# Optimization experiments

Hardware: AMD Instinct MI355X
Metric: run time of the kernel (lower is better)

## Reference

```python
import jax, jax.numpy as jnp
import numpy as np

N = 3072      # num nodes in g
E = 3072      # num edges in g (= num nodes in line graph lg)
E_LG = 6144   # num edges in line graph
F_NODE = 64
F_EDGE = 64
H = 4         # num_heads


def _init_linear(key, fan_in, fan_out):
    k1, k2 = jax.random.split(key)
    bound = 1.0 / np.sqrt(fan_in).astype(np.float32)
    W = jax.random.uniform(k1, (fan_in, fan_out), minval=-bound, maxval=bound, dtype=jnp.float32)
    b = jax.random.uniform(k2, (fan_out,), minval=-bound, maxval=bound, dtype=jnp.float32)
    return W, b


def setup_inputs() -> dict:
    key = jax.random.key(0)
    ks = jax.random.split(key, 12)
    node_inputs = jax.random.normal(ks[0], (N, F_NODE), dtype=jnp.float32)
    edge_inputs = jax.random.normal(ks[1], (E, F_EDGE), dtype=jnp.float32)
    src = jax.random.randint(ks[2], (E,), 0, N)
    dst = jax.random.randint(ks[3], (E,), 0, N)
    lg_src = jax.random.randint(ks[4], (E_LG,), 0, E)
    lg_dst = jax.random.randint(ks[5], (E_LG,), 0, E)
    nqW, nqb = _init_linear(ks[6], F_NODE, H * F_NODE)
    nkW, nkb = _init_linear(ks[7], F_NODE, H)
    nvW, nvb = _init_linear(ks[8], F_NODE, H * F_NODE)
    eqW, eqb = _init_linear(ks[9], F_EDGE, H * F_EDGE)
    ekW, ekb = _init_linear(ks[10], F_EDGE, H)
    evW, evb = _init_linear(ks[11], F_EDGE, H * F_EDGE)
    return dict(node_inputs=node_inputs, edge_inputs=edge_inputs,
                src=src, dst=dst, lg_src=lg_src, lg_dst=lg_dst,
                nqW=nqW, nqb=nqb, nkW=nkW, nkb=nkb, nvW=nvW, nvb=nvb,
                eqW=eqW, eqb=eqb, ekW=ekW, ekb=ekb, evW=evW, evb=evb)


def _self_attention(query, key_t, feats, short_residual):
    # query [H,M,F], key_t [H,M,1], short_residual [M,F]
    # original: softmax((q @ sr^T @ k) / sqrt(F), dim=1)
    # associate as q @ (sr^T @ k) to avoid an [H,M,M] intermediate
    srk = jnp.einsum('mf,hmo->hfo', short_residual, key_t)          # [H,F,1]
    x = jnp.einsum('hmf,hfo->hmo', query, srk) / np.float32(np.sqrt(feats))
    return jax.nn.softmax(x, axis=1)                                 # [H,M,1]


def reference(node_inputs, edge_inputs, src, dst, lg_src, lg_dst,
              nqW, nqb, nkW, nkb, nvW, nvb, eqW, eqb, ekW, ekb, evW, evb):
    # linear projections; torch .view(H,-1,F) on a row-major [M,H*F] tensor
    # is exactly jnp.reshape((H, M, F))
    node_q = (node_inputs @ nqW + nqb).reshape(H, N, F_NODE)
    node_k = (node_inputs @ nkW + nkb).reshape(H, N, 1)
    node_v = (node_inputs @ nvW + nvb).reshape(H, N, F_NODE)
    edge_q = (edge_inputs @ eqW + eqb).reshape(H, E, F_EDGE)
    edge_k = (edge_inputs @ ekW + ekb).reshape(H, E, 1)
    edge_v = (edge_inputs @ evW + evb).reshape(H, E, F_EDGE)

    node_att = _self_attention(node_q, node_k, F_NODE, node_inputs)  # [H,N,1]
    edge_att = _self_attention(edge_q, edge_k, F_EDGE, edge_inputs)  # [H,E,1]

    # scatter per-edge attention scores into dense [H,N,N]
    node_proj = jnp.zeros((H, N, N), jnp.float32).at[:, src, dst].set(edge_att[:, :, 0])
    # line-graph edge e1 -> e2 passes through connecting node dst[e1]
    conn = dst[lg_src]                                               # [E_LG]
    edge_proj = jnp.zeros((H, E, E), jnp.float32).at[:, lg_src, lg_dst].set(node_att[:, conn, 0])

    # dense adjacency masks
    adj_g = jnp.zeros((N, N), jnp.float32).at[src, dst].set(1.0)
    adj_lg = jnp.zeros((E, E), jnp.float32).at[lg_src, lg_dst].set(1.0)

    # message passing, aggregation='sum': (proj * adj) @ value
    node_msg = jnp.einsum('hnm,hmf->hnf', node_proj * adj_g, node_v)   # [H,N,F]
    edge_msg = jnp.einsum('hnm,hmf->hnf', edge_proj * adj_lg, edge_v)  # [H,E,F]

    # head pooling 'mean' (dropout p=0 => identity)
    return node_msg.mean(axis=0), edge_msg.mean(axis=0)
```

## Files before the change

### kernel.cpp

```cpp
#include <hip/hip_runtime.h>

#define N_NODES 3072
#define N_EDGES 3072
#define N_LG    6144
#define F       64
#define H       4
#define HASH_SZ 16384
#define HASH_MASK (HASH_SZ - 1)

#define OFF_PV   0
#define OFF_SRK  (OFF_PV + 2*H*N_NODES*F)
#define OFF_ATT  (OFF_SRK + 2*H*F)
#define OFF_HASH (OFF_ATT + 2*H*N_NODES)

__global__ __launch_bounds__(256) void init_kernel(
    float4* __restrict__ out, int4* __restrict__ hash, float* __restrict__ srk)
{
    const int b = blockIdx.x, t = threadIdx.x;
    if (b < 384) {
        out[b * 256 + t] = make_float4(0.f, 0.f, 0.f, 0.f);
    } else if (b < 448) {
        const int idx = (b - 384) * 256 + t;
        hash[idx] = (idx < 8192) ? make_int4(-1, -1, -1, -1) : make_int4(0, 0, 0, 0);
    } else {
        srk[t] = 0.f;
        srk[t + 256] = 0.f;
    }
}

__device__ __forceinline__ unsigned hash_slot(unsigned key) {
    return (key * 2654435761u >> 16) & HASH_MASK;
}

__global__ __launch_bounds__(256) void hash_insert_kernel(
    const int* __restrict__ src, const int* __restrict__ dst,
    const int* __restrict__ lg_src, const int* __restrict__ lg_dst,
    unsigned* __restrict__ keys_g, int* __restrict__ vals_g,
    unsigned* __restrict__ keys_lg, int* __restrict__ vals_lg)
{
    int b = blockIdx.x;
    const int* s; const int* d; unsigned* keys; int* vals; int n;
    if (b < 12) { s = src;    d = dst;    keys = keys_g;  vals = vals_g;  n = N_EDGES; }
    else { b -= 12; s = lg_src; d = lg_dst; keys = keys_lg; vals = vals_lg; n = N_LG; }
    const int e = b * 256 + threadIdx.x;
    if (e >= n) return;
    const unsigned key = (unsigned)(s[e] * N_NODES + d[e]);
    unsigned idx = hash_slot(key);
    while (true) {
        unsigned prev = atomicCAS(&keys[idx], 0xFFFFFFFFu, key);
        if (prev == 0xFFFFFFFFu || prev == key) { atomicMax(&vals[idx], e); break; }
        idx = (idx + 1) & HASH_MASK;
    }
}

__device__ __forceinline__ int hash_is_winner(
    unsigned key, const unsigned* __restrict__ keys, const int* __restrict__ vals, int e)
{
    unsigned idx = hash_slot(key);
    while (keys[idx] != key) idx = (idx + 1) & HASH_MASK;
    return vals[idx] == e;
}

__global__ __launch_bounds__(256) void srk_kernel(
    const float* __restrict__ node_in, const float* __restrict__ edge_in,
    const float* __restrict__ nkW, const float* __restrict__ nkb,
    const float* __restrict__ ekW, const float* __restrict__ ekb,
    float* __restrict__ srk)
{
    const int kind = blockIdx.y, b = blockIdx.x, t = threadIdx.x;
    const int h = b / 12, m0 = (b % 12) * 256, r0 = b * 64;
    const float* in = kind ? edge_in : node_in;
    const float* Wk = kind ? ekW : nkW;
    const float* bk = kind ? ekb : nkb;
    __shared__ float sin_[64 * 68];
    __shared__ float k_lds[256];
    __shared__ float wk_s[256];
    __shared__ float bk_s[4];
    #pragma unroll
    for (int i = 0; i < 4; ++i) {
        const int idx = t + i * 256;
        const int m = idx >> 4, q = idx & 15;
        float4 v = ((const float4*)(in + (size_t)(r0 + m) * F))[q];
        *(float4*)&sin_[m * 68 + q * 4] = v;
    }
    wk_s[t] = Wk[t];
    if (t < 4) bk_s[t] = bk[t];
    __syncthreads();
    {
        const int rl = t >> 2, c = t & 3;
        float acc = bk_s[c];
        #pragma unroll
        for (int j = 0; j < F; ++j) acc += sin_[rl * 68 + j] * wk_s[j * 4 + c];
        k_lds[t] = acc;
    }
    __syncthreads();
    {
        const int c = t >> 6, f = t & 63;
        float acc = 0.f;
        const float* base = in + (size_t)(m0 + c * 64) * F + f;
        #pragma unroll
        for (int mp = 0; mp < 64; ++mp) acc += base[(size_t)mp * F] * k_lds[c * 64 + mp];
        atomicAdd(&srk[(kind * H + h) * F + f], acc);
    }
}

__global__ __launch_bounds__(1024) void att_kernel(
    const float* __restrict__ node_in, const float* __restrict__ edge_in,
    const float* __restrict__ nqW, const float* __restrict__ nqb,
    const float* __restrict__ eqW, const float* __restrict__ eqb,
    float* __restrict__ ws)
{
    const int h = blockIdx.x, kind = blockIdx.y, tid = threadIdx.x;
    const float* in = kind ? edge_in : node_in;
    const float* Wq = kind ? eqW : nqW;
    const float* bq = kind ? eqb : nqb;
    float* att = ws + OFF_ATT + (kind * H + h) * N_NODES;
    __shared__ float s_srk[F];
    __shared__ float s_w[256];
    __shared__ float s_beff[4];
    __shared__ float sred[16];
    if (tid < F) s_srk[tid] = ws[OFF_SRK + (kind * H + h) * F + tid];
    __syncthreads();
    if (tid < 256) {
        const int c4 = tid >> 6, j = tid & 63;
        float we = 0.f;
        #pragma unroll
        for (int f = 0; f < F; ++f) we += Wq[j * 256 + c4 * 64 + f] * s_srk[f];
        s_w[c4 * 64 + j] = we;
    } else if (tid < 260) {
        const int c4 = tid - 256;
        float be = 0.f;
        #pragma unroll
        for (int f = 0; f < F; ++f) be += bq[c4 * 64 + f] * s_srk[f];
        s_beff[c4] = be;
    }
    __syncthreads();
    float x[3];
    float mx = -1e30f;
    #pragma unroll
    for (int j = 0; j < 3; ++j) {
        const int m = tid * 3 + j;
        const int row = h * 768 + (m >> 2);
        const int c4 = m & 3;
        const float4* q4 = (const float4*)(in + (size_t)row * F);
        const float* w = s_w + c4 * 64;
        float a = 0.f;
        #pragma unroll
        for (int i = 0; i < 16; ++i) {
            float4 v = q4[i];
            a += v.x * w[i * 4] + v.y * w[i * 4 + 1] + v.z * w[i * 4 + 2] + v.w * w[i * 4 + 3];
        }
        x[j] = (a + s_beff[c4]) * 0.125f;
        mx = fmaxf(mx, x[j]);
    }
    #pragma unroll
    for (int o = 1; o < 64; o <<= 1) mx = fmaxf(mx, __shfl_xor(mx, o));
    const int wid = tid >> 6, lane = tid & 63;
    if (lane == 0) sred[wid] = mx;
    __syncthreads();
    if (tid == 0) { float m2 = sred[0]; for (int i = 1; i < 16; ++i) m2 = fmaxf(m2, sred[i]); sred[0] = m2; }
    __syncthreads();
    mx = sred[0];
    __syncthreads();
    float s = 0.f;
    #pragma unroll
    for (int j = 0; j < 3; ++j) { x[j] = __expf(x[j] - mx); s += x[j]; }
    #pragma unroll
    for (int o = 1; o < 64; o <<= 1) s += __shfl_xor(s, o);
    if (lane == 0) sred[wid] = s;
    __syncthreads();
    if (tid == 0) { float t = 0.f; for (int i = 0; i < 16; ++i) t += sred[i]; sred[0] = t; }
    __syncthreads();
    const float inv = 1.0f / sred[0];
    #pragma unroll
    for (int j = 0; j < 3; ++j) att[tid * 3 + j] = x[j] * inv;
}

__global__ __launch_bounds__(256) void proj_v_kernel(
    const float* __restrict__ node_in, const float* __restrict__ edge_in,
    const float* __restrict__ nvW, const float* __restrict__ nvb,
    const float* __restrict__ evW, const float* __restrict__ evb,
    float* __restrict__ ws)
{
    const int kind = blockIdx.y, col = threadIdx.x;
    const int m0 = blockIdx.x * 32;
    const float* in = kind ? edge_in : node_in;
    const float* W  = kind ? evW : nvW;
    const float* bv = kind ? evb : nvb;
    __shared__ float sin_[32 * 68];
    #pragma unroll
    for (int i = 0; i < 2; ++i) {
        const int idx = col + i * 256;
        const int m = idx >> 4, q = idx & 15;
        float4 v = ((const float4*)(in + (size_t)(m0 + m) * F))[q];
        *(float4*)&sin_[m * 68 + q * 4] = v;
    }
    __syncthreads();
    float acc[32];
    const float b0 = bv[col];
    #pragma unroll
    for (int r = 0; r < 32; ++r) acc[r] = b0;
    #pragma unroll
    for (int k4 = 0; k4 < 16; ++k4) {
        const float w0 = W[(k4 * 4 + 0) * 256 + col];
        const float w1 = W[(k4 * 4 + 1) * 256 + col];
        const float w2 = W[(k4 * 4 + 2) * 256 + col];
        const float w3 = W[(k4 * 4 + 3) * 256 + col];
        #pragma unroll
        for (int r = 0; r < 32; ++r) {
            float4 v = *(const float4*)&sin_[r * 68 + k4 * 4];
            acc[r] = fmaf(v.x, w0, fmaf(v.y, w1, fmaf(v.z, w2, fmaf(v.w, w3, acc[r]))));
        }
    }
    float* V = ws + OFF_PV + (size_t)kind * H * N_NODES * F;
    #pragma unroll
    for (int r = 0; r < 32; ++r)
        V[(size_t)(m0 + r) * 256 + col] = acc[r];
}

__global__ __launch_bounds__(64) void scatter_kernel(
    const int* __restrict__ src, const int* __restrict__ dst,
    const int* __restrict__ lg_src, const int* __restrict__ lg_dst,
    const float* __restrict__ ws,
    const unsigned* __restrict__ keys_g, const int* __restrict__ vals_g,
    const unsigned* __restrict__ keys_lg, const int* __restrict__ vals_lg,
    float* __restrict__ out)
{
    const int b = blockIdx.x;
    const int f = threadIdx.x;
    if (b < N_EDGES) {
        const int e = b;
        const int s = src[e], d = dst[e];
        const unsigned key = (unsigned)(s * N_NODES + d);
        if (!hash_is_winner(key, keys_g, vals_g, e)) return;
        const float* att = ws + OFF_ATT + H * N_NODES;
        const float* V   = ws + OFF_PV;
        float acc = 0.f;
        #pragma unroll
        for (int h = 0; h < H; ++h)
            acc += att[h * N_EDGES + e] * V[(size_t)h * N_NODES * F + (size_t)d * F + f];
        atomicAdd(&out[s * F + f], 0.25f * acc);
    } else {
        const int l = b - N_EDGES;
        const int e1 = lg_src[l], e2 = lg_dst[l];
        const unsigned key = (unsigned)(e1 * N_NODES + e2);
        if (!hash_is_winner(key, keys_lg, vals_lg, l)) return;
        const int conn = dst[e1];
        const float* att = ws + OFF_ATT;
        const float* V   = ws + OFF_PV + (size_t)H * N_EDGES * F;
        float acc = 0.f;
        #pragma unroll
        for (int h = 0; h < H; ++h)
            acc += att[h * N_NODES + conn] * V[(size_t)h * N_EDGES * F + (size_t)e2 * F + f];
        atomicAdd(&out[N_NODES * F + e1 * F + f], 0.25f * acc);
    }
}

extern "C" void kernel_launch(void* const* d_in, const int* in_sizes, int n_in,
                              void* d_out, int out_size, void* d_ws, size_t ws_size,
                              hipStream_t stream)
{
    const float* node_in = (const float*)d_in[0];
    const float* edge_in = (const float*)d_in[1];
    const int* src    = (const int*)d_in[2];
    const int* dst    = (const int*)d_in[3];
    const int* lg_src = (const int*)d_in[4];
    const int* lg_dst = (const int*)d_in[5];
    const float* nqW = (const float*)d_in[6];  const float* nqb = (const float*)d_in[7];
    const float* nkW = (const float*)d_in[8];  const float* nkb = (const float*)d_in[9];
    const float* nvW = (const float*)d_in[10]; const float* nvb = (const float*)d_in[11];
    const float* eqW = (const float*)d_in[12]; const float* eqb = (const float*)d_in[13];
    const float* ekW = (const float*)d_in[14]; const float* ekb = (const float*)d_in[15];
    const float* evW = (const float*)d_in[16]; const float* evb = (const float*)d_in[17];

    float* ws  = (float*)d_ws;
    float* out = (float*)d_out;
    unsigned* keys_g  = (unsigned*)(ws + OFF_HASH);
    unsigned* keys_lg = keys_g + HASH_SZ;
    int* vals_g  = (int*)(keys_g + 2 * HASH_SZ);
    int* vals_lg = vals_g + HASH_SZ;

    hipLaunchKernelGGL(init_kernel, dim3(449), dim3(256), 0, stream,
                       (float4*)out, (int4*)(ws + OFF_HASH), ws + OFF_SRK);
    hipLaunchKernelGGL(hash_insert_kernel, dim3(36), dim3(256), 0, stream,
                       src, dst, lg_src, lg_dst, keys_g, vals_g, keys_lg, vals_lg);
    hipLaunchKernelGGL(srk_kernel, dim3(48, 2), dim3(256), 0, stream,
                       node_in, edge_in, nkW, nkb, ekW, ekb, ws + OFF_SRK);
    hipLaunchKernelGGL(att_kernel, dim3(H, 2), dim3(1024), 0, stream,
                       node_in, edge_in, nqW, nqb, eqW, eqb, ws);
    hipLaunchKernelGGL(proj_v_kernel, dim3(96, 2), dim3(256), 0, stream,
                       node_in, edge_in, nvW, nvb, evW, evb, ws);
    hipLaunchKernelGGL(scatter_kernel, dim3(N_EDGES + N_LG), dim3(64), 0, stream,
                       src, dst, lg_src, lg_dst, ws, keys_g, vals_g, keys_lg, vals_lg, out);
}
```

Before: 150.8 us.

## Fuse all stages into one cooperative persistent kernel with grid syncs

```diff
diff --git a/kernel.cpp b/kernel.cpp
--- a/kernel.cpp
+++ b/kernel.cpp
@@ -1,4 +1,7 @@
 #include <hip/hip_runtime.h>
+#include <hip/hip_cooperative_groups.h>
+
+namespace cg = cooperative_groups;
 
 #define N_NODES 3072
 #define N_EDGES 3072
@@ -13,44 +16,10 @@
 #define OFF_ATT  (OFF_SRK + 2*H*F)
 #define OFF_HASH (OFF_ATT + 2*H*N_NODES)
 
-__global__ __launch_bounds__(256) void init_kernel(
-    float4* __restrict__ out, int4* __restrict__ hash, float* __restrict__ srk)
-{
-    const int b = blockIdx.x, t = threadIdx.x;
-    if (b < 384) {
-        out[b * 256 + t] = make_float4(0.f, 0.f, 0.f, 0.f);
-    } else if (b < 448) {
-        const int idx = (b - 384) * 256 + t;
-        hash[idx] = (idx < 8192) ? make_int4(-1, -1, -1, -1) : make_int4(0, 0, 0, 0);
-    } else {
-        srk[t] = 0.f;
-        srk[t + 256] = 0.f;
-    }
-}
+#define NBLK 256
 
 __device__ __forceinline__ unsigned hash_slot(unsigned key) {
     return (key * 2654435761u >> 16) & HASH_MASK;
-}
-
-__global__ __launch_bounds__(256) void hash_insert_kernel(
-    const int* __restrict__ src, const int* __restrict__ dst,
-    const int* __restrict__ lg_src, const int* __restrict__ lg_dst,
-    unsigned* __restrict__ keys_g, int* __restrict__ vals_g,
-    unsigned* __restrict__ keys_lg, int* __restrict__ vals_lg)
-{
-    int b = blockIdx.x;
-    const int* s; const int* d; unsigned* keys; int* vals; int n;
-    if (b < 12) { s = src;    d = dst;    keys = keys_g;  vals = vals_g;  n = N_EDGES; }
-    else { b -= 12; s = lg_src; d = lg_dst; keys = keys_lg; vals = vals_lg; n = N_LG; }
-    const int e = b * 256 + threadIdx.x;
-    if (e >= n) return;
-    const unsigned key = (unsigned)(s[e] * N_NODES + d[e]);
-    unsigned idx = hash_slot(key);
-    while (true) {
-        unsigned prev = atomicCAS(&keys[idx], 0xFFFFFFFFu, key);
-        if (prev == 0xFFFFFFFFu || prev == key) { atomicMax(&vals[idx], e); break; }
-        idx = (idx + 1) & HASH_MASK;
-    }
 }
 
 __device__ __forceinline__ int hash_is_winner(
@@ -61,198 +30,233 @@
     return vals[idx] == e;
 }
 
-__global__ __launch_bounds__(256) void srk_kernel(
+#define L_SIN   0
+#define L_KL    4352
+#define L_WK    4608
+#define L_BK    4864
+#define L_RED   4868
+#define LDS_FLOATS (L_RED + 16)
+
+__global__ __launch_bounds__(256) void mega_kernel(
     const float* __restrict__ node_in, const float* __restrict__ edge_in,
-    const float* __restrict__ nkW, const float* __restrict__ nkb,
-    const float* __restrict__ ekW, const float* __restrict__ ekb,
-    float* __restrict__ srk)
-{
-    const int kind = blockIdx.y, b = blockIdx.x, t = threadIdx.x;
-    const int h = b / 12, m0 = (b % 12) * 256, r0 = b * 64;
-    const float* in = kind ? edge_in : node_in;
-    const float* Wk = kind ? ekW : nkW;
-    const float* bk = kind ? ekb : nkb;
-    __shared__ float sin_[64 * 68];
-    __shared__ float k_lds[256];
-    __shared__ float wk_s[256];
-    __shared__ float bk_s[4];
-    #pragma unroll
-    for (int i = 0; i < 4; ++i) {
-        const int idx = t + i * 256;
-        const int m = idx >> 4, q = idx & 15;
-        float4 v = ((const float4*)(in + (size_t)(r0 + m) * F))[q];
-        *(float4*)&sin_[m * 68 + q * 4] = v;
-    }
-    wk_s[t] = Wk[t];
-    if (t < 4) bk_s[t] = bk[t];
-    __syncthreads();
-    {
-        const int rl = t >> 2, c = t & 3;
-        float acc = bk_s[c];
-        #pragma unroll
-        for (int j = 0; j < F; ++j) acc += sin_[rl * 68 + j] * wk_s[j * 4 + c];
-        k_lds[t] = acc;
-    }
-    __syncthreads();
-    {
-        const int c = t >> 6, f = t & 63;
-        float acc = 0.f;
-        const float* base = in + (size_t)(m0 + c * 64) * F + f;
-        #pragma unroll
-        for (int mp = 0; mp < 64; ++mp) acc += base[(size_t)mp * F] * k_lds[c * 64 + mp];
-        atomicAdd(&srk[(kind * H + h) * F + f], acc);
-    }
-}
-
-__global__ __launch_bounds__(1024) void att_kernel(
-    const float* __restrict__ node_in, const float* __restrict__ edge_in,
-    const float* __restrict__ nqW, const float* __restrict__ nqb,
-    const float* __restrict__ eqW, const float* __restrict__ eqb,
-    float* __restrict__ ws)
-{
-    const int h = blockIdx.x, kind = blockIdx.y, tid = threadIdx.x;
-    const float* in = kind ? edge_in : node_in;
-    const float* Wq = kind ? eqW : nqW;
-    const float* bq = kind ? eqb : nqb;
-    float* att = ws + OFF_ATT + (kind * H + h) * N_NODES;
-    __shared__ float s_srk[F];
-    __shared__ float s_w[256];
-    __shared__ float s_beff[4];
-    __shared__ float sred[16];
-    if (tid < F) s_srk[tid] = ws[OFF_SRK + (kind * H + h) * F + tid];
-    __syncthreads();
-    if (tid < 256) {
-        const int c4 = tid >> 6, j = tid & 63;
-        float we = 0.f;
-        #pragma unroll
-        for (int f = 0; f < F; ++f) we += Wq[j * 256 + c4 * 64 + f] * s_srk[f];
-        s_w[c4 * 64 + j] = we;
-    } else if (tid < 260) {
-        const int c4 = tid - 256;
-        float be = 0.f;
-        #pragma unroll
-        for (int f = 0; f < F; ++f) be += bq[c4 * 64 + f] * s_srk[f];
-        s_beff[c4] = be;
-    }
-    __syncthreads();
-    float x[3];
-    float mx = -1e30f;
-    #pragma unroll
-    for (int j = 0; j < 3; ++j) {
-        const int m = tid * 3 + j;
-        const int row = h * 768 + (m >> 2);
-        const int c4 = m & 3;
-        const float4* q4 = (const float4*)(in + (size_t)row * F);
-        const float* w = s_w + c4 * 64;
-        float a = 0.f;
-        #pragma unroll
-        for (int i = 0; i < 16; ++i) {
-            float4 v = q4[i];
-            a += v.x * w[i * 4] + v.y * w[i * 4 + 1] + v.z * w[i * 4 + 2] + v.w * w[i * 4 + 3];
-        }
-        x[j] = (a + s_beff[c4]) * 0.125f;
-        mx = fmaxf(mx, x[j]);
-    }
-    #pragma unroll
-    for (int o = 1; o < 64; o <<= 1) mx = fmaxf(mx, __shfl_xor(mx, o));
-    const int wid = tid >> 6, lane = tid & 63;
-    if (lane == 0) sred[wid] = mx;
-    __syncthreads();
-    if (tid == 0) { float m2 = sred[0]; for (int i = 1; i < 16; ++i) m2 = fmaxf(m2, sred[i]); sred[0] = m2; }
-    __syncthreads();
-    mx = sred[0];
-    __syncthreads();
-    float s = 0.f;
-    #pragma unroll
-    for (int j = 0; j < 3; ++j) { x[j] = __expf(x[j] - mx); s += x[j]; }
-    #pragma unroll
-    for (int o = 1; o < 64; o <<= 1) s += __shfl_xor(s, o);
-    if (lane == 0) sred[wid] = s;
-    __syncthreads();
-    if (tid == 0) { float t = 0.f; for (int i = 0; i < 16; ++i) t += sred[i]; sred[0] = t; }
-    __syncthreads();
-    const float inv = 1.0f / sred[0];
-    #pragma unroll
-    for (int j = 0; j < 3; ++j) att[tid * 3 + j] = x[j] * inv;
-}
-
-__global__ __launch_bounds__(256) void proj_v_kernel(
-    const float* __restrict__ node_in, const float* __restrict__ edge_in,
-    const float* __restrict__ nvW, const float* __restrict__ nvb,
-    const float* __restrict__ evW, const float* __restrict__ evb,
-    float* __restrict__ ws)
-{
-    const int kind = blockIdx.y, col = threadIdx.x;
-    const int m0 = blockIdx.x * 32;
-    const float* in = kind ? edge_in : node_in;
-    const float* W  = kind ? evW : nvW;
-    const float* bv = kind ? evb : nvb;
-    __shared__ float sin_[32 * 68];
-    #pragma unroll
-    for (int i = 0; i < 2; ++i) {
-        const int idx = col + i * 256;
-        const int m = idx >> 4, q = idx & 15;
-        float4 v = ((const float4*)(in + (size_t)(m0 + m) * F))[q];
-        *(float4*)&sin_[m * 68 + q * 4] = v;
-    }
-    __syncthreads();
-    float acc[32];
-    const float b0 = bv[col];
-    #pragma unroll
-    for (int r = 0; r < 32; ++r) acc[r] = b0;
-    #pragma unroll
-    for (int k4 = 0; k4 < 16; ++k4) {
-        const float w0 = W[(k4 * 4 + 0) * 256 + col];
-        const float w1 = W[(k4 * 4 + 1) * 256 + col];
-        const float w2 = W[(k4 * 4 + 2) * 256 + col];
-        const float w3 = W[(k4 * 4 + 3) * 256 + col];
-        #pragma unroll
-        for (int r = 0; r < 32; ++r) {
-            float4 v = *(const float4*)&sin_[r * 68 + k4 * 4];
-            acc[r] = fmaf(v.x, w0, fmaf(v.y, w1, fmaf(v.z, w2, fmaf(v.w, w3, acc[r]))));
-        }
-    }
-    float* V = ws + OFF_PV + (size_t)kind * H * N_NODES * F;
-    #pragma unroll
-    for (int r = 0; r < 32; ++r)
-        V[(size_t)(m0 + r) * 256 + col] = acc[r];
-}
-
-__global__ __launch_bounds__(64) void scatter_kernel(
     const int* __restrict__ src, const int* __restrict__ dst,
     const int* __restrict__ lg_src, const int* __restrict__ lg_dst,
-    const float* __restrict__ ws,
-    const unsigned* __restrict__ keys_g, const int* __restrict__ vals_g,
-    const unsigned* __restrict__ keys_lg, const int* __restrict__ vals_lg,
-    float* __restrict__ out)
+    const float* __restrict__ nqW, const float* __restrict__ nqb,
+    const float* __restrict__ nkW, const float* __restrict__ nkb,
+    const float* __restrict__ nvW, const float* __restrict__ nvb,
+    const float* __restrict__ eqW, const float* __restrict__ eqb,
+    const float* __restrict__ ekW, const float* __restrict__ ekb,
+    const float* __restrict__ evW, const float* __restrict__ evb,
+    float* __restrict__ ws, float* __restrict__ out)
 {
-    const int b = blockIdx.x;
-    const int f = threadIdx.x;
-    if (b < N_EDGES) {
-        const int e = b;
-        const int s = src[e], d = dst[e];
-        const unsigned key = (unsigned)(s * N_NODES + d);
-        if (!hash_is_winner(key, keys_g, vals_g, e)) return;
-        const float* att = ws + OFF_ATT + H * N_NODES;
-        const float* V   = ws + OFF_PV;
-        float acc = 0.f;
-        #pragma unroll
-        for (int h = 0; h < H; ++h)
-            acc += att[h * N_EDGES + e] * V[(size_t)h * N_NODES * F + (size_t)d * F + f];
-        atomicAdd(&out[s * F + f], 0.25f * acc);
+    cg::grid_group grid = cg::this_grid();
+    const int b = blockIdx.x, t = threadIdx.x;
+    const int gtid = b * 256 + t;
+    __shared__ float lds[LDS_FLOATS];
+
+    unsigned* keys_g  = (unsigned*)(ws + OFF_HASH);
+    unsigned* keys_lg = keys_g + HASH_SZ;
+    int* vals_g  = (int*)(keys_g + 2 * HASH_SZ);
+    int* vals_lg = vals_g + HASH_SZ;
+
+    {
+        float4* out4 = (float4*)out;
+        if (gtid < 98304) out4[gtid] = make_float4(0.f, 0.f, 0.f, 0.f);
+        const int i2 = gtid + 65536;
+        if (i2 < 98304) out4[i2] = make_float4(0.f, 0.f, 0.f, 0.f);
+        int4* hash4 = (int4*)(ws + OFF_HASH);
+        if (gtid < 16384) hash4[gtid] = (gtid < 8192) ? make_int4(-1, -1, -1, -1) : make_int4(0, 0, 0, 0);
+        if (gtid < 512) ws[OFF_SRK + gtid] = 0.f;
+    }
+    grid.sync();
+
+    if (b < 96) {
+        const int tile = b % 48, kind = b / 48;
+        const int h = tile / 12, m0 = (tile % 12) * 256, r0 = tile * 64;
+        const float* in = kind ? edge_in : node_in;
+        const float* Wk = kind ? ekW : nkW;
+        const float* bk = kind ? ekb : nkb;
+        float* sin_ = lds + L_SIN;
+        float* k_lds = lds + L_KL;
+        float* wk_s = lds + L_WK;
+        float* bk_s = lds + L_BK;
+        #pragma unroll
+        for (int i = 0; i < 4; ++i) {
+            const int idx = t + i * 256;
+            const int m = idx >> 4, q = idx & 15;
+            float4 v = ((const float4*)(in + (size_t)(r0 + m) * F))[q];
+            *(float4*)&sin_[m * 68 + q * 4] = v;
+        }
+        wk_s[t] = Wk[t];
+        if (t < 4) bk_s[t] = bk[t];
+        __syncthreads();
+        {
+            const int rl = t >> 2, c = t & 3;
+            float acc = bk_s[c];
+            #pragma unroll
+            for (int j = 0; j < F; ++j) acc += sin_[rl * 68 + j] * wk_s[j * 4 + c];
+            k_lds[t] = acc;
+        }
+        __syncthreads();
+        {
+            const int c = t >> 6, f = t & 63;
+            float acc = 0.f;
+            const float* base = in + (size_t)(m0 + c * 64) * F + f;
+            #pragma unroll
+            for (int mp = 0; mp < 64; ++mp) acc += base[(size_t)mp * F] * k_lds[c * 64 + mp];
+            atomicAdd(&ws[OFF_SRK + (kind * H + h) * F + f], acc);
+        }
     } else {
-        const int l = b - N_EDGES;
-        const int e1 = lg_src[l], e2 = lg_dst[l];
-        const unsigned key = (unsigned)(e1 * N_NODES + e2);
-        if (!hash_is_winner(key, keys_lg, vals_lg, l)) return;
-        const int conn = dst[e1];
-        const float* att = ws + OFF_ATT;
-        const float* V   = ws + OFF_PV + (size_t)H * N_EDGES * F;
-        float acc = 0.f;
-        #pragma unroll
-        for (int h = 0; h < H; ++h)
-            acc += att[h * N_NODES + conn] * V[(size_t)h * N_EDGES * F + (size_t)e2 * F + f];
-        atomicAdd(&out[N_NODES * F + e1 * F + f], 0.25f * acc);
+        float* sin_ = lds + L_SIN;
+        const int ntask = (b < 128) ? 2 : 1;
+        for (int it = 0; it < ntask; ++it) {
+            const int p = (it == 0) ? (b - 96) : (b - 96 + 160);
+            const int kind = p / 96, m0 = (p % 96) * 32;
+            const float* in = kind ? edge_in : node_in;
+            const float* W  = kind ? evW : nvW;
+            const float* bv = kind ? evb : nvb;
+            if (it) __syncthreads();
+            #pragma unroll
+            for (int i = 0; i < 2; ++i) {
+                const int idx = t + i * 256;
+                const int m = idx >> 4, q = idx & 15;
+                float4 v = ((const float4*)(in + (size_t)(m0 + m) * F))[q];
+                *(float4*)&sin_[m * 68 + q * 4] = v;
+            }
+            __syncthreads();
+            float acc[32];
+            const float b0 = bv[t];
+            #pragma unroll
+            for (int r = 0; r < 32; ++r) acc[r] = b0;
+            #pragma unroll
+            for (int k4 = 0; k4 < 16; ++k4) {
+                const float w0 = W[(k4 * 4 + 0) * 256 + t];
+                const float w1 = W[(k4 * 4 + 1) * 256 + t];
+                const float w2 = W[(k4 * 4 + 2) * 256 + t];
+                const float w3 = W[(k4 * 4 + 3) * 256 + t];
+                #pragma unroll
+                for (int r = 0; r < 32; ++r) {
+                    float4 v = *(const float4*)&sin_[r * 68 + k4 * 4];
+                    acc[r] = fmaf(v.x, w0, fmaf(v.y, w1, fmaf(v.z, w2, fmaf(v.w, w3, acc[r]))));
+                }
+            }
+            float* V = ws + OFF_PV + (size_t)kind * H * N_NODES * F;
+            #pragma unroll
+            for (int r = 0; r < 32; ++r)
+                V[(size_t)(m0 + r) * 256 + t] = acc[r];
+        }
+        if (b >= 220) {
+            int q = b - 220;
+            const int* s; const int* d; unsigned* keys; int* vals; int n; int e0;
+            if (q < 12) { s = src;    d = dst;    keys = keys_g;  vals = vals_g;  n = N_EDGES; e0 = q * 256; }
+            else { s = lg_src; d = lg_dst; keys = keys_lg; vals = vals_lg; n = N_LG; e0 = (q - 12) * 256; }
+            const int e = e0 + t;
+            if (e < n) {
+                const unsigned key = (unsigned)(s[e] * N_NODES + d[e]);
+                unsigned idx = hash_slot(key);
+                while (true) {
+                    unsigned prev = atomicCAS(&keys[idx], 0xFFFFFFFFu, key);
+                    if (prev == 0xFFFFFFFFu || prev == key) { atomicMax(&vals[idx], e); break; }
+                    idx = (idx + 1) & HASH_MASK;
+                }
+            }
+        }
+    }
+    grid.sync();
+
+    if (b < 8) {
+        const int h = b & 3, kind = b >> 2;
+        const float* in = kind ? edge_in : node_in;
+        const float* Wq = kind ? eqW : nqW;
+        const float* bq = kind ? eqb : nqb;
+        float* att = ws + OFF_ATT + (kind * H + h) * N_NODES;
+        float* s_srk = lds + L_SIN;
+        float* s_w   = lds + L_SIN + 64;
+        float* s_beff = lds + L_SIN + 320;
+        float* sred  = lds + L_RED;
+        if (t < 64) s_srk[t] = ws[OFF_SRK + (kind * H + h) * F + t];
+        __syncthreads();
+        {
+            const int c4 = t >> 6, j = t & 63;
+            float we = 0.f;
+            #pragma unroll
+            for (int f = 0; f < F; ++f) we += Wq[j * 256 + c4 * 64 + f] * s_srk[f];
+            s_w[c4 * 64 + j] = we;
+        }
+        if (t < 4) {
+            float be = 0.f;
+            #pragma unroll
+            for (int f = 0; f < F; ++f) be += bq[t * 64 + f] * s_srk[f];
+            s_beff[t] = be;
+        }
+        __syncthreads();
+        float x[12];
+        float mx = -1e30f;
+        #pragma unroll
+        for (int j = 0; j < 12; ++j) {
+            const int m = t + 256 * j;
+            const int row = h * 768 + (m >> 2);
+            const int c4 = m & 3;
+            const float4* q4 = (const float4*)(in + (size_t)row * F);
+            const float* w = s_w + c4 * 64;
+            float a = 0.f;
+            #pragma unroll
+            for (int i = 0; i < 16; ++i) {
+                float4 v = q4[i];
+                a += v.x * w[i * 4] + v.y * w[i * 4 + 1] + v.z * w[i * 4 + 2] + v.w * w[i * 4 + 3];
+            }
+            x[j] = (a + s_beff[c4]) * 0.125f;
+            mx = fmaxf(mx, x[j]);
+        }
+        const int wid = t >> 6, lane = t & 63;
+        #pragma unroll
+        for (int o = 1; o < 64; o <<= 1) mx = fmaxf(mx, __shfl_xor(mx, o));
+        if (lane == 0) sred[wid] = mx;
+        __syncthreads();
+        mx = fmaxf(fmaxf(sred[0], sred[1]), fmaxf(sred[2], sred[3]));
+        float s = 0.f;
+        #pragma unroll
+        for (int j = 0; j < 12; ++j) { x[j] = __expf(x[j] - mx); s += x[j]; }
+        #pragma unroll
+        for (int o = 1; o < 64; o <<= 1) s += __shfl_xor(s, o);
+        if (lane == 0) sred[4 + wid] = s;
+        __syncthreads();
+        const float inv = 1.0f / (sred[4] + sred[5] + sred[6] + sred[7]);
+        #pragma unroll
+        for (int j = 0; j < 12; ++j) att[t + 256 * j] = x[j] * inv;
+    }
+    grid.sync();
+
+    {
+        const int g = t >> 6, f = t & 63;
+        for (int task = b * 4 + g; task < N_EDGES + N_LG; task += NBLK * 4) {
+            if (task < N_EDGES) {
+                const int e = task;
+                const int s = src[e], d = dst[e];
+                const unsigned key = (unsigned)(s * N_NODES + d);
+                if (!hash_is_winner(key, keys_g, vals_g, e)) continue;
+                const float* att = ws + OFF_ATT + H * N_NODES;
+                const float* V   = ws + OFF_PV;
+                float acc = 0.f;
+                #pragma unroll
+                for (int h = 0; h < H; ++h)
+                    acc += att[h * N_EDGES + e] * V[(size_t)h * N_NODES * F + (size_t)d * F + f];
+                atomicAdd(&out[s * F + f], 0.25f * acc);
+            } else {
+                const int l = task - N_EDGES;
+                const int e1 = lg_src[l], e2 = lg_dst[l];
+                const unsigned key = (unsigned)(e1 * N_NODES + e2);
+                if (!hash_is_winner(key, keys_lg, vals_lg, l)) continue;
+                const int conn = dst[e1];
+                const float* att = ws + OFF_ATT;
+                const float* V   = ws + OFF_PV + (size_t)H * N_EDGES * F;
+                float acc = 0.f;
+                #pragma unroll
+                for (int h = 0; h < H; ++h)
+                    acc += att[h * N_NODES + conn] * V[(size_t)h * N_EDGES * F + (size_t)e2 * F + f];
+                atomicAdd(&out[N_NODES * F + e1 * F + f], 0.25f * acc);
+            }
+        }
     }
 }
 
@@ -275,21 +279,14 @@
 
     float* ws  = (float*)d_ws;
     float* out = (float*)d_out;
-    unsigned* keys_g  = (unsigned*)(ws + OFF_HASH);
-    unsigned* keys_lg = keys_g + HASH_SZ;
-    int* vals_g  = (int*)(keys_g + 2 * HASH_SZ);
-    int* vals_lg = vals_g + HASH_SZ;
-
-    hipLaunchKernelGGL(init_kernel, dim3(449), dim3(256), 0, stream,
-                       (float4*)out, (int4*)(ws + OFF_HASH), ws + OFF_SRK);
-    hipLaunchKernelGGL(hash_insert_kernel, dim3(36), dim3(256), 0, stream,
-                       src, dst, lg_src, lg_dst, keys_g, vals_g, keys_lg, vals_lg);
-    hipLaunchKernelGGL(srk_kernel, dim3(48, 2), dim3(256), 0, stream,
-                       node_in, edge_in, nkW, nkb, ekW, ekb, ws + OFF_SRK);
-    hipLaunchKernelGGL(att_kernel, dim3(H, 2), dim3(1024), 0, stream,
-                       node_in, edge_in, nqW, nqb, eqW, eqb, ws);
-    hipLaunchKernelGGL(proj_v_kernel, dim3(96, 2), dim3(256), 0, stream,
-                       node_in, edge_in, nvW, nvb, evW, evb, ws);
-    hipLaunchKernelGGL(scatter_kernel, dim3(N_EDGES + N_LG), dim3(64), 0, stream,
-                       src, dst, lg_src, lg_dst, ws, keys_g, vals_g, keys_lg, vals_lg, out);
-}
+
+    void* args[] = {
+        (void*)&node_in, (void*)&edge_in, (void*)&src, (void*)&dst,
+        (void*)&lg_src, (void*)&lg_dst,
+        (void*)&nqW, (void*)&nqb, (void*)&nkW, (void*)&nkb, (void*)&nvW, (void*)&nvb,
+        (void*)&eqW, (void*)&eqb, (void*)&ekW, (void*)&ekb, (void*)&evW, (void*)&evb,
+        (void*)&ws, (void*)&out
+    };
+    hipLaunchCooperativeKernel((const void*)mega_kernel, dim3(NBLK), dim3(256),
+                               args, 0, stream);
+}
```

Result: slower. 244.8 us (+62.4%).

## Fuse hash insert, srk and V projection into one launch; pack scatter tasks

Applied to the files above, without the earlier changes.

```diff
diff --git a/kernel.cpp b/kernel.cpp
--- a/kernel.cpp
+++ b/kernel.cpp
@@ -12,6 +12,18 @@
 #define OFF_SRK  (OFF_PV + 2*H*N_NODES*F)
 #define OFF_ATT  (OFF_SRK + 2*H*F)
 #define OFF_HASH (OFF_ATT + 2*H*N_NODES)
+
+__device__ __forceinline__ unsigned hash_slot(unsigned key) {
+    return (key * 2654435761u >> 16) & HASH_MASK;
+}
+
+__device__ __forceinline__ int hash_is_winner(
+    unsigned key, const unsigned* __restrict__ keys, const int* __restrict__ vals, int e)
+{
+    unsigned idx = hash_slot(key);
+    while (keys[idx] != key) idx = (idx + 1) & HASH_MASK;
+    return vals[idx] == e;
+}
 
 __global__ __launch_bounds__(256) void init_kernel(
     float4* __restrict__ out, int4* __restrict__ hash, float* __restrict__ srk)
@@ -28,79 +40,115 @@
     }
 }
 
-__device__ __forceinline__ unsigned hash_slot(unsigned key) {
-    return (key * 2654435761u >> 16) & HASH_MASK;
-}
-
-__global__ __launch_bounds__(256) void hash_insert_kernel(
+#define L_SIN   0
+#define L_KL    4352
+#define L_WK    4608
+#define L_BK    4864
+#define LDS_FLOATS (L_BK + 4)
+
+__global__ __launch_bounds__(256) void phase1_kernel(
+    const float* __restrict__ node_in, const float* __restrict__ edge_in,
     const int* __restrict__ src, const int* __restrict__ dst,
     const int* __restrict__ lg_src, const int* __restrict__ lg_dst,
-    unsigned* __restrict__ keys_g, int* __restrict__ vals_g,
-    unsigned* __restrict__ keys_lg, int* __restrict__ vals_lg)
-{
-    int b = blockIdx.x;
-    const int* s; const int* d; unsigned* keys; int* vals; int n;
-    if (b < 12) { s = src;    d = dst;    keys = keys_g;  vals = vals_g;  n = N_EDGES; }
-    else { b -= 12; s = lg_src; d = lg_dst; keys = keys_lg; vals = vals_lg; n = N_LG; }
-    const int e = b * 256 + threadIdx.x;
-    if (e >= n) return;
-    const unsigned key = (unsigned)(s[e] * N_NODES + d[e]);
-    unsigned idx = hash_slot(key);
-    while (true) {
-        unsigned prev = atomicCAS(&keys[idx], 0xFFFFFFFFu, key);
-        if (prev == 0xFFFFFFFFu || prev == key) { atomicMax(&vals[idx], e); break; }
-        idx = (idx + 1) & HASH_MASK;
-    }
-}
-
-__device__ __forceinline__ int hash_is_winner(
-    unsigned key, const unsigned* __restrict__ keys, const int* __restrict__ vals, int e)
-{
-    unsigned idx = hash_slot(key);
-    while (keys[idx] != key) idx = (idx + 1) & HASH_MASK;
-    return vals[idx] == e;
-}
-
-__global__ __launch_bounds__(256) void srk_kernel(
-    const float* __restrict__ node_in, const float* __restrict__ edge_in,
     const float* __restrict__ nkW, const float* __restrict__ nkb,
     const float* __restrict__ ekW, const float* __restrict__ ekb,
-    float* __restrict__ srk)
-{
-    const int kind = blockIdx.y, b = blockIdx.x, t = threadIdx.x;
-    const int h = b / 12, m0 = (b % 12) * 256, r0 = b * 64;
-    const float* in = kind ? edge_in : node_in;
-    const float* Wk = kind ? ekW : nkW;
-    const float* bk = kind ? ekb : nkb;
-    __shared__ float sin_[64 * 68];
-    __shared__ float k_lds[256];
-    __shared__ float wk_s[256];
-    __shared__ float bk_s[4];
-    #pragma unroll
-    for (int i = 0; i < 4; ++i) {
-        const int idx = t + i * 256;
-        const int m = idx >> 4, q = idx & 15;
-        float4 v = ((const float4*)(in + (size_t)(r0 + m) * F))[q];
-        *(float4*)&sin_[m * 68 + q * 4] = v;
-    }
-    wk_s[t] = Wk[t];
-    if (t < 4) bk_s[t] = bk[t];
-    __syncthreads();
-    {
-        const int rl = t >> 2, c = t & 3;
-        float acc = bk_s[c];
-        #pragma unroll
-        for (int j = 0; j < F; ++j) acc += sin_[rl * 68 + j] * wk_s[j * 4 + c];
-        k_lds[t] = acc;
-    }
-    __syncthreads();
-    {
-        const int c = t >> 6, f = t & 63;
-        float acc = 0.f;
-        const float* base = in + (size_t)(m0 + c * 64) * F + f;
-        #pragma unroll
-        for (int mp = 0; mp < 64; ++mp) acc += base[(size_t)mp * F] * k_lds[c * 64 + mp];
-        atomicAdd(&srk[(kind * H + h) * F + f], acc);
+    const float* __restrict__ nvW, const float* __restrict__ nvb,
+    const float* __restrict__ evW, const float* __restrict__ evb,
+    float* __restrict__ ws)
+{
+    const int b = blockIdx.x, t = threadIdx.x;
+    __shared__ float lds[LDS_FLOATS];
+
+    if (b < 96) {
+        const int tile = b % 48, kind = b / 48;
+        const int h = tile / 12, m0 = (tile % 12) * 256, r0 = tile * 64;
+        const float* in = kind ? edge_in : node_in;
+        const float* Wk = kind ? ekW : nkW;
+        const float* bk = kind ? ekb : nkb;
+        float* sin_ = lds + L_SIN;
+        float* k_lds = lds + L_KL;
+        float* wk_s = lds + L_WK;
+        float* bk_s = lds + L_BK;
+        #pragma unroll
+        for (int i = 0; i < 4; ++i) {
+            const int idx = t + i * 256;
+            const int m = idx >> 4, q = idx & 15;
+            float4 v = ((const float4*)(in + (size_t)(r0 + m) * F))[q];
+            *(float4*)&sin_[m * 68 + q * 4] = v;
+        }
+        wk_s[t] = Wk[t];
+        if (t < 4) bk_s[t] = bk[t];
+        __syncthreads();
+        {
+            const int rl = t >> 2, c = t & 3;
+            float acc = bk_s[c];
+            #pragma unroll
+            for (int j = 0; j < F; ++j) acc += sin_[rl * 68 + j] * wk_s[j * 4 + c];
+            k_lds[t] = acc;
+        }
+        __syncthreads();
+        {
+            const int c = t >> 6, f = t & 63;
+            float acc = 0.f;
+            const float* base = in + (size_t)(m0 + c * 64) * F + f;
+            #pragma unroll
+            for (int mp = 0; mp < 64; ++mp) acc += base[(size_t)mp * F] * k_lds[c * 64 + mp];
+            atomicAdd(&ws[OFF_SRK + (kind * H + h) * F + f], acc);
+        }
+    } else if (b < 288) {
+        const int p = b - 96;
+        const int kind = p / 96, m0 = (p % 96) * 32;
+        const float* in = kind ? edge_in : node_in;
+        const float* W  = kind ? evW : nvW;
+        const float* bv = kind ? evb : nvb;
+        float* sin_ = lds + L_SIN;
+        #pragma unroll
+        for (int i = 0; i < 2; ++i) {
+            const int idx = t + i * 256;
+            const int m = idx >> 4, q = idx & 15;
+            float4 v = ((const float4*)(in + (size_t)(m0 + m) * F))[q];
+            *(float4*)&sin_[m * 68 + q * 4] = v;
+        }
+        __syncthreads();
+        float acc[32];
+        const float b0 = bv[t];
+        #pragma unroll
+        for (int r = 0; r < 32; ++r) acc[r] = b0;
+        #pragma unroll
+        for (int k4 = 0; k4 < 16; ++k4) {
+            const float w0 = W[(k4 * 4 + 0) * 256 + t];
+            const float w1 = W[(k4 * 4 + 1) * 256 + t];
+            const float w2 = W[(k4 * 4 + 2) * 256 + t];
+            const float w3 = W[(k4 * 4 + 3) * 256 + t];
+            #pragma unroll
+            for (int r = 0; r < 32; ++r) {
+                float4 v = *(const float4*)&sin_[r * 68 + k4 * 4];
+                acc[r] = fmaf(v.x, w0, fmaf(v.y, w1, fmaf(v.z, w2, fmaf(v.w, w3, acc[r]))));
+            }
+        }
+        float* V = ws + OFF_PV + (size_t)kind * H * N_NODES * F;
+        #pragma unroll
+        for (int r = 0; r < 32; ++r)
+            V[(size_t)(m0 + r) * 256 + t] = acc[r];
+    } else {
+        unsigned* keys_g  = (unsigned*)(ws + OFF_HASH);
+        unsigned* keys_lg = keys_g + HASH_SZ;
+        int* vals_g  = (int*)(keys_g + 2 * HASH_SZ);
+        int* vals_lg = vals_g + HASH_SZ;
+        int q = b - 288;
+        const int* s; const int* d; unsigned* keys; int* vals; int n; int e0;
+        if (q < 12) { s = src;    d = dst;    keys = keys_g;  vals = vals_g;  n = N_EDGES; e0 = q * 256; }
+        else { s = lg_src; d = lg_dst; keys = keys_lg; vals = vals_lg; n = N_LG; e0 = (q - 12) * 256; }
+        const int e = e0 + t;
+        if (e < n) {
+            const unsigned key = (unsigned)(s[e] * N_NODES + d[e]);
+            unsigned idx = hash_slot(key);
+            while (true) {
+                unsigned prev = atomicCAS(&keys[idx], 0xFFFFFFFFu, key);
+                if (prev == 0xFFFFFFFFu || prev == key) { atomicMax(&vals[idx], e); break; }
+                idx = (idx + 1) & HASH_MASK;
+            }
+        }
     }
 }
 
@@ -176,60 +224,20 @@
     for (int j = 0; j < 3; ++j) att[tid * 3 + j] = x[j] * inv;
 }
 
-__global__ __launch_bounds__(256) void proj_v_kernel(
-    const float* __restrict__ node_in, const float* __restrict__ edge_in,
-    const float* __restrict__ nvW, const float* __restrict__ nvb,
-    const float* __restrict__ evW, const float* __restrict__ evb,
-    float* __restrict__ ws)
-{
-    const int kind = blockIdx.y, col = threadIdx.x;
-    const int m0 = blockIdx.x * 32;
-    const float* in = kind ? edge_in : node_in;
-    const float* W  = kind ? evW : nvW;
-    const float* bv = kind ? evb : nvb;
-    __shared__ float sin_[32 * 68];
-    #pragma unroll
-    for (int i = 0; i < 2; ++i) {
-        const int idx = col + i * 256;
-        const int m = idx >> 4, q = idx & 15;
-        float4 v = ((const float4*)(in + (size_t)(m0 + m) * F))[q];
-        *(float4*)&sin_[m * 68 + q * 4] = v;
-    }
-    __syncthreads();
-    float acc[32];
-    const float b0 = bv[col];
-    #pragma unroll
-    for (int r = 0; r < 32; ++r) acc[r] = b0;
-    #pragma unroll
-    for (int k4 = 0; k4 < 16; ++k4) {
-        const float w0 = W[(k4 * 4 + 0) * 256 + col];
-        const float w1 = W[(k4 * 4 + 1) * 256 + col];
-        const float w2 = W[(k4 * 4 + 2) * 256 + col];
-        const float w3 = W[(k4 * 4 + 3) * 256 + col];
-        #pragma unroll
-        for (int r = 0; r < 32; ++r) {
-            float4 v = *(const float4*)&sin_[r * 68 + k4 * 4];
-            acc[r] = fmaf(v.x, w0, fmaf(v.y, w1, fmaf(v.z, w2, fmaf(v.w, w3, acc[r]))));
-        }
-    }
-    float* V = ws + OFF_PV + (size_t)kind * H * N_NODES * F;
-    #pragma unroll
-    for (int r = 0; r < 32; ++r)
-        V[(size_t)(m0 + r) * 256 + col] = acc[r];
-}
-
-__global__ __launch_bounds__(64) void scatter_kernel(
+__global__ __launch_bounds__(256) void scatter_kernel(
     const int* __restrict__ src, const int* __restrict__ dst,
     const int* __restrict__ lg_src, const int* __restrict__ lg_dst,
     const float* __restrict__ ws,
-    const unsigned* __restrict__ keys_g, const int* __restrict__ vals_g,
-    const unsigned* __restrict__ keys_lg, const int* __restrict__ vals_lg,
     float* __restrict__ out)
 {
-    const int b = blockIdx.x;
-    const int f = threadIdx.x;
-    if (b < N_EDGES) {
-        const int e = b;
+    const unsigned* keys_g  = (const unsigned*)(ws + OFF_HASH);
+    const unsigned* keys_lg = keys_g + HASH_SZ;
+    const int* vals_g  = (const int*)(keys_g + 2 * HASH_SZ);
+    const int* vals_lg = vals_g + HASH_SZ;
+    const int g = threadIdx.x >> 6, f = threadIdx.x & 63;
+    const int task = blockIdx.x * 4 + g;
+    if (task < N_EDGES) {
+        const int e = task;
         const int s = src[e], d = dst[e];
         const unsigned key = (unsigned)(s * N_NODES + d);
         if (!hash_is_winner(key, keys_g, vals_g, e)) return;
@@ -241,7 +249,7 @@
             acc += att[h * N_EDGES + e] * V[(size_t)h * N_NODES * F + (size_t)d * F + f];
         atomicAdd(&out[s * F + f], 0.25f * acc);
     } else {
-        const int l = b - N_EDGES;
+        const int l = task - N_EDGES;
         const int e1 = lg_src[l], e2 = lg_dst[l];
         const unsigned key = (unsigned)(e1 * N_NODES + e2);
         if (!hash_is_winner(key, keys_lg, vals_lg, l)) return;
@@ -275,21 +283,14 @@
 
     float* ws  = (float*)d_ws;
     float* out = (float*)d_out;
-    unsigned* keys_g  = (unsigned*)(ws + OFF_HASH);
-    unsigned* keys_lg = keys_g + HASH_SZ;
-    int* vals_g  = (int*)(keys_g + 2 * HASH_SZ);
-    int* vals_lg = vals_g + HASH_SZ;
 
     hipLaunchKernelGGL(init_kernel, dim3(449), dim3(256), 0, stream,
                        (float4*)out, (int4*)(ws + OFF_HASH), ws + OFF_SRK);
-    hipLaunchKernelGGL(hash_insert_kernel, dim3(36), dim3(256), 0, stream,
-                       src, dst, lg_src, lg_dst, keys_g, vals_g, keys_lg, vals_lg);
-    hipLaunchKernelGGL(srk_kernel, dim3(48, 2), dim3(256), 0, stream,
-                       node_in, edge_in, nkW, nkb, ekW, ekb, ws + OFF_SRK);
+    hipLaunchKernelGGL(phase1_kernel, dim3(324), dim3(256), 0, stream,
+                       node_in, edge_in, src, dst, lg_src, lg_dst,
+                       nkW, nkb, ekW, ekb, nvW, nvb, evW, evb, ws);
     hipLaunchKernelGGL(att_kernel, dim3(H, 2), dim3(1024), 0, stream,
                        node_in, edge_in, nqW, nqb, eqW, eqb, ws);
-    hipLaunchKernelGGL(proj_v_kernel, dim3(96, 2), dim3(256), 0, stream,
-                       node_in, edge_in, nvW, nvb, evW, evb, ws);
-    hipLaunchKernelGGL(scatter_kernel, dim3(N_EDGES + N_LG), dim3(64), 0, stream,
-                       src, dst, lg_src, lg_dst, ws, keys_g, vals_g, keys_lg, vals_lg, out);
-}
+    hipLaunchKernelGGL(scatter_kernel, dim3((N_EDGES + N_LG) / 4), dim3(256), 0, stream,
+                       src, dst, lg_src, lg_dst, ws, out);
+}
```

Result: faster. 140.2 us (-7.0%).
